# Performance work log

Hardware: AMD Instinct MI355X
Metric: run time of the kernel (lower is better)

## Reference

```python
import jax, jax.numpy as jnp
import numpy as np

N_NODES = 100000
N_EDGES = 1600000
N_GRAPHS = 1000
H = 128
F_IN = 128
F_EDGE = 16
DEPTH = 4


def setup_inputs() -> dict:
    key = jax.random.key(0)
    ks = jax.random.split(key, 10)
    s = 1.0 / np.sqrt(H)
    x = jax.random.normal(ks[0], (N_NODES, F_IN), dtype=jnp.float32)
    edge_index = jax.random.randint(ks[1], (2, N_EDGES), 0, N_NODES, dtype=jnp.int32)
    edge_attr = jax.random.normal(ks[2], (N_EDGES, F_EDGE), dtype=jnp.float32)
    batch = jnp.sort(jax.random.randint(ks[3], (N_NODES,), 0, N_GRAPHS, dtype=jnp.int32))
    W0 = jax.random.normal(ks[4], (F_IN, H), dtype=jnp.float32) * s
    b0 = jnp.zeros((H,), dtype=jnp.float32)
    W1 = jax.random.normal(ks[5], (DEPTH, H, H), dtype=jnp.float32) * s
    b1 = jnp.zeros((DEPTH, H), dtype=jnp.float32)
    W2 = jax.random.normal(ks[6], (DEPTH, H, H), dtype=jnp.float32) * s
    b2 = jnp.zeros((DEPTH, H), dtype=jnp.float32)
    Wf = jax.random.normal(ks[7], (H, 1), dtype=jnp.float32) * s
    bf = jnp.zeros((1,), dtype=jnp.float32)
    return {"x": x, "edge_index": edge_index, "edge_attr": edge_attr, "batch": batch,
            "W0": W0, "b0": b0, "W1": W1, "b1": b1, "W2": W2, "b2": b2, "Wf": Wf, "bf": bf}


def reference(x, edge_index, edge_attr, batch, W0, b0, W1, b1, W2, b2, Wf, bf):
    # edge_attr is read by the original forward but never used in the math.
    src, dst = edge_index[0], edge_index[1]
    n = x.shape[0]
    h0 = jax.nn.relu(x @ W0 + b0)  # [N, H]
    h = h0
    for i in range(DEPTH):
        # GINConv (eps=0): MLP(x + sum_{j in N(i)} x_j); messages flow src -> dst
        agg = jax.ops.segment_sum(h[src], dst, num_segments=n)  # [N, H]
        z = h + agg
        z = jax.nn.relu(z @ W1[i] + b1[i]) @ W2[i] + b2[i]
        # residual then relu (dropout p=0.02 is identity at eval)
        h = jax.nn.relu(z + h0)
    pooled = jax.ops.segment_sum(h, batch, num_segments=N_GRAPHS)  # [G, H]
    out = (pooled @ Wf + bf)[:, 0]  # [G]
    return out
```

## Files before the change

### kernel.cpp

```cpp
#include <hip/hip_runtime.h>

#define N_NODES 100000
#define N_EDGES 1600000
#define N_GRAPHS 1000
#define H 128
#define DEPTH 4
#define NB 391
#define BCAP 4864
#define WPITCH 136
#define WSLOT (H * WPITCH)

typedef __attribute__((ext_vector_type(8))) short bf16x8;
typedef __attribute__((ext_vector_type(4))) float f32x4;
typedef __attribute__((ext_vector_type(4))) unsigned int u32x4;

__device__ __forceinline__ unsigned short f2bf(float f) {
  unsigned int u = __float_as_uint(f);
  u += 0x7FFF + ((u >> 16) & 1);
  return (unsigned short)(u >> 16);
}
__device__ __forceinline__ float bflo(unsigned int v) { return __uint_as_float(v << 16); }
__device__ __forceinline__ float bfhi(unsigned int v) { return __uint_as_float(v & 0xFFFF0000u); }

__global__ __launch_bounds__(512) void k_bscan(const int* __restrict__ gcnt, int* __restrict__ boff) {
  __shared__ int sh[512];
  int t = threadIdx.x;
  int v = (t < NB) ? gcnt[t] : 0;
  sh[t] = v;
  __syncthreads();
  for (int s = 1; s < 512; s <<= 1) {
    int x = (t >= s) ? sh[t - s] : 0;
    __syncthreads();
    sh[t] += x;
    __syncthreads();
  }
  if (t < NB) boff[t] = sh[t] - v;
  if (t == 0) boff[NB] = N_EDGES;
}

__global__ __launch_bounds__(256) void k_bucket(const int* __restrict__ src, const int* __restrict__ dst,
                                                int* __restrict__ gcnt, unsigned int* __restrict__ ebuf) {
  __shared__ int cnt[NB];
  __shared__ int base[NB];
  int tid = threadIdx.x;
  int e0 = blockIdx.x * 4096;
  for (int i = tid; i < NB; i += 256) cnt[i] = 0;
  __syncthreads();
  unsigned int pk[16];
  int bk[16], rk[16];
#pragma unroll
  for (int i = 0; i < 16; ++i) {
    int e = e0 + i * 256 + tid;
    if (e < N_EDGES) {
      int s = src[e], d = dst[e];
      bk[i] = d >> 8;
      pk[i] = ((unsigned int)(d & 255) << 17) | (unsigned int)s;
      rk[i] = atomicAdd(&cnt[bk[i]], 1);
    } else
      bk[i] = -1;
  }
  __syncthreads();
  for (int i = tid; i < NB; i += 256)
    base[i] = cnt[i] ? atomicAdd(&gcnt[i], cnt[i]) : 0;
  __syncthreads();
#pragma unroll
  for (int i = 0; i < 16; ++i)
    if (bk[i] >= 0) ebuf[(size_t)bk[i] * BCAP + base[bk[i]] + rk[i]] = pk[i];
}

__global__ __launch_bounds__(256) void k_bsort(const unsigned int* __restrict__ ebuf,
                                               const int* __restrict__ gcnt, const int* __restrict__ boff,
                                               int* __restrict__ csr, int* __restrict__ offs) {
  __shared__ unsigned int arr[BCAP];
  __shared__ unsigned int srt[BCAP];
  __shared__ unsigned short rnk[BCAP];
  __shared__ int cnt[256];
  __shared__ int off[257];
  int b = blockIdx.x, tid = threadIdx.x;
  int beg = boff[b];
  int ce = min(gcnt[b], BCAP);
  cnt[tid] = 0;
  __syncthreads();
  for (int i = tid; i < ce; i += 256) {
    unsigned int p = ebuf[(size_t)b * BCAP + i];
    arr[i] = p;
    rnk[i] = (unsigned short)atomicAdd(&cnt[p >> 17], 1);
  }
  __syncthreads();
  int v = cnt[tid];
  off[tid + 1] = v;
  if (tid == 0) off[0] = 0;
  __syncthreads();
  for (int s = 1; s < 256; s <<= 1) {
    int x = (tid + 1 > s) ? off[tid + 1 - s] : 0;
    __syncthreads();
    off[tid + 1] += x;
    __syncthreads();
  }
  for (int i = tid; i < ce; i += 256) {
    unsigned int p = arr[i];
    srt[off[p >> 17] + rnk[i]] = p & 0x1FFFF;
  }
  __syncthreads();
  for (int i = tid; i < ce; i += 256) csr[beg + i] = (int)srt[i];
  int node = (b << 8) + tid;
  if (node < N_NODES) offs[node] = beg + off[tid];
  if (b == NB - 1 && tid == 0) offs[N_NODES] = N_EDGES;
}

__global__ __launch_bounds__(256) void k_wprep(const float* __restrict__ W0, const float* __restrict__ W1,
                                               const float* __restrict__ W2, unsigned short* __restrict__ wb) {
  int m = blockIdx.x >> 3, part = blockIdx.x & 7, tid = threadIdx.x;
  const float* src = (m == 0) ? W0 : ((m <= DEPTH) ? W1 + (size_t)(m - 1) * H * H : W2 + (size_t)(m - 1 - DEPTH) * H * H);
  unsigned short* dst = wb + (size_t)m * WSLOT;
  int idx = part * 256 + tid;
  int ng4 = idx & 31, kp = idx >> 5;
  float4 r0 = *(const float4*)&src[(2 * kp) * H + 4 * ng4];
  float4 r1 = *(const float4*)&src[(2 * kp + 1) * H + 4 * ng4];
  unsigned int p0 = (unsigned int)f2bf(r0.x) | ((unsigned int)f2bf(r1.x) << 16);
  unsigned int p1 = (unsigned int)f2bf(r0.y) | ((unsigned int)f2bf(r1.y) << 16);
  unsigned int p2 = (unsigned int)f2bf(r0.z) | ((unsigned int)f2bf(r1.z) << 16);
  unsigned int p3 = (unsigned int)f2bf(r0.w) | ((unsigned int)f2bf(r1.w) << 16);
  *(unsigned int*)&dst[(4 * ng4 + 0) * WPITCH + 2 * kp] = p0;
  *(unsigned int*)&dst[(4 * ng4 + 1) * WPITCH + 2 * kp] = p1;
  *(unsigned int*)&dst[(4 * ng4 + 2) * WPITCH + 2 * kp] = p2;
  *(unsigned int*)&dst[(4 * ng4 + 3) * WPITCH + 2 * kp] = p3;
}

__device__ __forceinline__ void stage_wb(const unsigned short* __restrict__ Wg, unsigned short* Wt, int tid) {
#pragma unroll
  for (int i = 0; i < 4; ++i) {
    int c = tid + i * 512;
    *(uint4*)&Wt[c * 8] = *(const uint4*)&Wg[c * 8];
  }
  int c = tid + 2048;
  if (c < 2176) *(uint4*)&Wt[c * 8] = *(const uint4*)&Wg[c * 8];
}

__global__ __launch_bounds__(512, 4) void k_lin(const float* __restrict__ in, const unsigned short* __restrict__ w0t,
                                                const float* __restrict__ bg, unsigned short* __restrict__ outp) {
  __shared__ __align__(16) unsigned short Wt[WSLOT];
  __shared__ __align__(16) unsigned short zs[128 * 136];
  int tid = threadIdx.x;
  int lane = tid & 63, w = tid >> 6;
  int q = lane >> 4, l16 = lane & 15;
  int n0 = blockIdx.x * 128;

  stage_wb(w0t, Wt, tid);

  int row = n0 + w * 16 + l16;
  int rr = (row < N_NODES) ? row : 0;
  bf16x8 afrag[4];
#pragma unroll
  for (int ks = 0; ks < 4; ++ks) {
    const float* p = &in[(size_t)rr * H + ks * 32 + q * 8];
    f32x4 f0 = __builtin_nontemporal_load((const f32x4*)p);
    f32x4 f1 = __builtin_nontemporal_load((const f32x4*)(p + 4));
    bf16x8 a;
    a[0] = (short)f2bf(f0.x); a[1] = (short)f2bf(f0.y); a[2] = (short)f2bf(f0.z); a[3] = (short)f2bf(f0.w);
    a[4] = (short)f2bf(f1.x); a[5] = (short)f2bf(f1.y); a[6] = (short)f2bf(f1.z); a[7] = (short)f2bf(f1.w);
    afrag[ks] = a;
  }
  f32x4 acc[8];
#pragma unroll
  for (int ct = 0; ct < 8; ++ct) acc[ct] = (f32x4){0.f, 0.f, 0.f, 0.f};
  __syncthreads();
#pragma unroll
  for (int ct = 0; ct < 8; ++ct)
#pragma unroll
    for (int ks = 0; ks < 4; ++ks) {
      bf16x8 b = *(bf16x8*)&Wt[(ct * 16 + l16) * WPITCH + ks * 32 + q * 8];
      acc[ct] = __builtin_amdgcn_mfma_f32_16x16x32_bf16(afrag[ks], b, acc[ct], 0, 0, 0);
    }
#pragma unroll
  for (int ct = 0; ct < 8; ++ct) {
    float bb = bg[ct * 16 + l16];
#pragma unroll
    for (int r = 0; r < 4; ++r) {
      float v = fmaxf(acc[ct][r] + bb, 0.f);
      zs[(w * 16 + q * 4 + r) * 136 + ct * 16 + l16] = f2bf(v);
    }
  }
  __syncthreads();
  int node = tid >> 2, cb = (tid & 3) * 32;
  if (n0 + node < N_NODES) {
#pragma unroll
    for (int i = 0; i < 4; ++i) {
      uint4 v = *(uint4*)&zs[node * 136 + cb + i * 8];
      *(uint4*)&outp[(size_t)(n0 + node) * H + cb + i * 8] = v;
    }
  }
}

#define ACC8(v)                                                       \
  {                                                                   \
    a0 += bflo(v.x); a1 += bfhi(v.x); a2 += bflo(v.y); a3 += bfhi(v.y); \
    a4 += bflo(v.z); a5 += bfhi(v.z); a6 += bflo(v.w); a7 += bfhi(v.w); \
  }

__global__ __launch_bounds__(512, 4) void k_mlp(const unsigned short* __restrict__ hin,
                                                const int* __restrict__ offs, const int* __restrict__ csr,
                                                const unsigned short* __restrict__ w1t, const float* __restrict__ b1g,
                                                const unsigned short* __restrict__ w2t, const float* __restrict__ b2g,
                                                const unsigned short* __restrict__ h0, unsigned short* __restrict__ hout) {
  __shared__ __align__(16) unsigned short Wt[WSLOT];
  __shared__ __align__(16) unsigned short zs[128 * 136];
  int tid = threadIdx.x;
  int n0 = blockIdx.x * 128;

  stage_wb(w1t, Wt, tid);

  {
    int g = tid >> 4, l = tid & 15;
    const uint4* hu4 = (const uint4*)hin;
    int bn = n0 + g * 4;
    int ofs[5];
#pragma unroll
    for (int k = 0; k < 5; ++k) ofs[k] = offs[min(bn + k, N_NODES)];
    int idxp[4];
#pragma unroll
    for (int it = 0; it < 4; ++it)
      idxp[it] = (ofs[it] + l < ofs[it + 1]) ? csr[ofs[it] + l] : N_NODES;
#pragma unroll
    for (int it = 0; it < 4; ++it) {
      int nl = g * 4 + it;
      int nc = min(n0 + nl, N_NODES);
      uint4 self = hu4[(size_t)nc * 16 + l];
      float a0 = bflo(self.x), a1 = bfhi(self.x), a2 = bflo(self.y), a3 = bfhi(self.y);
      float a4 = bflo(self.z), a5 = bfhi(self.z), a6 = bflo(self.w), a7 = bfhi(self.w);
      int beg = ofs[it], end = ofs[it + 1];
      int idx = idxp[it];
      for (int e = beg; e < end; e += 16) {
        int en = e + 16;
        int idxn = (en + l < end) ? csr[en + l] : N_NODES;
        int s[16];
#pragma unroll
        for (int j = 0; j < 16; ++j) s[j] = __shfl(idx, j, 16);
        uint4 v[16];
#pragma unroll
        for (int j = 0; j < 16; ++j) v[j] = hu4[(size_t)s[j] * 16 + l];
#pragma unroll
        for (int j = 0; j < 16; ++j) { ACC8(v[j]) }
        idx = idxn;
      }
      unsigned int o0 = (unsigned int)f2bf(a0) | ((unsigned int)f2bf(a1) << 16);
      unsigned int o1 = (unsigned int)f2bf(a2) | ((unsigned int)f2bf(a3) << 16);
      unsigned int o2 = (unsigned int)f2bf(a4) | ((unsigned int)f2bf(a5) << 16);
      unsigned int o3 = (unsigned int)f2bf(a6) | ((unsigned int)f2bf(a7) << 16);
      uint4 o;
      o.x = o0; o.y = o1; o.z = o2; o.w = o3;
      *(uint4*)&zs[nl * 136 + l * 8] = o;
    }
  }
  __syncthreads();

  int lane = tid & 63, w = tid >> 6;
  int q = lane >> 4, l16 = lane & 15;
  bf16x8 afrag[4];
#pragma unroll
  for (int ks = 0; ks < 4; ++ks)
    afrag[ks] = *(bf16x8*)&zs[(w * 16 + l16) * 136 + ks * 32 + q * 8];

  f32x4 acc[8];
#pragma unroll
  for (int ct = 0; ct < 8; ++ct) acc[ct] = (f32x4){0.f, 0.f, 0.f, 0.f};
#pragma unroll
  for (int ct = 0; ct < 8; ++ct)
#pragma unroll
    for (int ks = 0; ks < 4; ++ks) {
      bf16x8 b = *(bf16x8*)&Wt[(ct * 16 + l16) * WPITCH + ks * 32 + q * 8];
      acc[ct] = __builtin_amdgcn_mfma_f32_16x16x32_bf16(afrag[ks], b, acc[ct], 0, 0, 0);
    }
  __syncthreads();
  stage_wb(w2t, Wt, tid);
#pragma unroll
  for (int ct = 0; ct < 8; ++ct) {
    float bb = b1g[ct * 16 + l16];
#pragma unroll
    for (int r = 0; r < 4; ++r) {
      float v = fmaxf(acc[ct][r] + bb, 0.f);
      zs[(w * 16 + q * 4 + r) * 136 + ct * 16 + l16] = f2bf(v);
    }
  }
  __syncthreads();

  bf16x8 a2[4];
#pragma unroll
  for (int ks = 0; ks < 4; ++ks)
    a2[ks] = *(bf16x8*)&zs[(w * 16 + l16) * 136 + ks * 32 + q * 8];
  f32x4 acc2[8];
#pragma unroll
  for (int ct = 0; ct < 8; ++ct) acc2[ct] = (f32x4){0.f, 0.f, 0.f, 0.f};
#pragma unroll
  for (int ct = 0; ct < 8; ++ct)
#pragma unroll
    for (int ks = 0; ks < 4; ++ks) {
      bf16x8 b = *(bf16x8*)&Wt[(ct * 16 + l16) * WPITCH + ks * 32 + q * 8];
      acc2[ct] = __builtin_amdgcn_mfma_f32_16x16x32_bf16(a2[ks], b, acc2[ct], 0, 0, 0);
    }
#pragma unroll
  for (int ct = 0; ct < 8; ++ct) {
    float bb = b2g[ct * 16 + l16];
#pragma unroll
    for (int r = 0; r < 4; ++r) {
      float v = acc2[ct][r] + bb;
      zs[(w * 16 + q * 4 + r) * 136 + ct * 16 + l16] = f2bf(v);
    }
  }
  __syncthreads();
  int node = tid >> 2, cb = (tid & 3) * 32;
  if (n0 + node < N_NODES) {
    size_t base = (size_t)(n0 + node) * H + cb;
#pragma unroll
    for (int i = 0; i < 4; ++i) {
      u32x4 zv = *(u32x4*)&zs[node * 136 + cb + i * 8];
      u32x4 hv = *(const u32x4*)&h0[base + i * 8];
      u32x4 o;
#pragma unroll
      for (int j = 0; j < 4; ++j) {
        float a = fmaxf(bflo(zv[j]) + bflo(hv[j]), 0.f);
        float b = fmaxf(bfhi(zv[j]) + bfhi(hv[j]), 0.f);
        o[j] = (unsigned int)f2bf(a) | ((unsigned int)f2bf(b) << 16);
      }
      *(u32x4*)&hout[base + i * 8] = o;
    }
  }
}

__global__ void k_starts(const int* __restrict__ batch, int* __restrict__ starts) {
  int n = blockIdx.x * 256 + threadIdx.x;
  if (n >= N_NODES) return;
  int b = batch[n];
  if (n == 0) {
    for (int g = 0; g <= b; ++g) starts[g] = 0;
  } else {
    int bp = batch[n - 1];
    for (int g = bp + 1; g <= b; ++g) starts[g] = n;
  }
  if (n == N_NODES - 1) {
    for (int g = b + 1; g <= N_GRAPHS; ++g) starts[g] = N_NODES;
  }
}

__global__ __launch_bounds__(256) void k_pool(const unsigned short* __restrict__ h, const int* __restrict__ starts,
                                              const float* __restrict__ Wf, const float* __restrict__ bf_,
                                              float* __restrict__ out) {
  __shared__ float r[4];
  int g = blockIdx.x, tid = threadIdx.x;
  int lane = tid & 63, w = tid >> 6;
  int beg = starts[g], end = starts[g + 1];
  const unsigned int* hu = (const unsigned int*)h;
  float sx = 0.f, sy = 0.f;
  for (int n = beg + w; n < end; n += 4) {
    unsigned int v = hu[(size_t)n * 64 + lane];
    sx += bflo(v);
    sy += bfhi(v);
  }
  float val = sx * Wf[2 * lane] + sy * Wf[2 * lane + 1];
#pragma unroll
  for (int off = 32; off > 0; off >>= 1) val += __shfl_down(val, off);
  if (lane == 0) r[w] = val;
  __syncthreads();
  if (tid == 0) out[g] = r[0] + r[1] + r[2] + r[3] + bf_[0];
}

extern "C" void kernel_launch(void* const* d_in, const int* in_sizes, int n_in,
                              void* d_out, int out_size, void* d_ws, size_t ws_size,
                              hipStream_t stream) {
  const float* x = (const float*)d_in[0];
  const int* ei = (const int*)d_in[1];
  const int* srcv = ei;
  const int* dstv = ei + N_EDGES;
  const int* batch = (const int*)d_in[3];
  const float* W0 = (const float*)d_in[4];
  const float* b0 = (const float*)d_in[5];
  const float* W1 = (const float*)d_in[6];
  const float* b1 = (const float*)d_in[7];
  const float* W2 = (const float*)d_in[8];
  const float* b2 = (const float*)d_in[9];
  const float* Wf = (const float*)d_in[10];
  const float* bf_ = (const float*)d_in[11];
  float* out = (float*)d_out;

  char* ws = (char*)d_ws;
  size_t o = 0;
  auto alloc = [&](size_t bytes) {
    size_t r = o;
    o = (o + bytes + 255) & ~(size_t)255;
    return r;
  };
  int* offs = (int*)(ws + alloc((N_NODES + 1) * sizeof(int)));
  int* gcnt = (int*)(ws + alloc(NB * sizeof(int)));
  int* boff = (int*)(ws + alloc((NB + 1) * sizeof(int)));
  unsigned int* ebuf = (unsigned int*)(ws + alloc((size_t)NB * BCAP * 4));
  int* csr = (int*)(ws + alloc((size_t)N_EDGES * sizeof(int)));
  int* starts = (int*)(ws + alloc((N_GRAPHS + 1) * sizeof(int)));
  unsigned short* h0 = (unsigned short*)(ws + alloc((size_t)(N_NODES + 1) * H * 2));
  unsigned short* hA = (unsigned short*)(ws + alloc((size_t)(N_NODES + 1) * H * 2));
  unsigned short* hB = (unsigned short*)(ws + alloc((size_t)(N_NODES + 1) * H * 2));
  unsigned short* wbuf = (unsigned short*)(ws + alloc((size_t)9 * WSLOT * 2));

  (void)hipMemsetAsync(gcnt, 0, NB * sizeof(int), stream);
  (void)hipMemsetAsync(h0 + (size_t)N_NODES * H, 0, H * 2, stream);
  (void)hipMemsetAsync(hA + (size_t)N_NODES * H, 0, H * 2, stream);
  (void)hipMemsetAsync(hB + (size_t)N_NODES * H, 0, H * 2, stream);
  k_wprep<<<72, 256, 0, stream>>>(W0, W1, W2, wbuf);
  k_bucket<<<NB, 256, 0, stream>>>(srcv, dstv, gcnt, ebuf);
  k_bscan<<<1, 512, 0, stream>>>(gcnt, boff);
  k_bsort<<<NB, 256, 0, stream>>>(ebuf, gcnt, boff, csr, offs);
  k_starts<<<(N_NODES + 255) / 256, 256, 0, stream>>>(batch, starts);

  const int nblk = (N_NODES + 127) / 128;
  k_lin<<<nblk, 512, 0, stream>>>(x, wbuf, b0, h0);
  for (int i = 0; i < DEPTH; ++i) {
    const unsigned short* hin = (i == 0) ? h0 : ((i & 1) ? hA : hB);
    unsigned short* hout = (i & 1) ? hB : hA;
    k_mlp<<<nblk, 512, 0, stream>>>(hin, offs, csr,
                                    wbuf + (size_t)(1 + i) * WSLOT, b1 + (size_t)i * H,
                                    wbuf + (size_t)(1 + DEPTH + i) * WSLOT, b2 + (size_t)i * H,
                                    h0, hout);
  }
  k_pool<<<N_GRAPHS, 256, 0, stream>>>(hB, starts, Wf, bf_, out);
}
```

Measured before the change: 575.9 us.

## Split node features into column slices and separate aggregation from MLP kernel

Node feature buffers are stored as 8 column slices of 16 bf16 each, and neighbor aggregation moves into a separate k_agg kernel. Each k_agg block handles one slice for 64 nodes, so the gathered working set per slice (about 3.2 MB) can stay in cache across random neighbor reads. The MLP kernel then reads the aggregated z from global memory. This adds an extra round-trip of z through memory per layer and extra kernel launches, and gather reads shrink to 8 bytes per lane.

```diff
diff --git a/kernel.cpp b/kernel.cpp
--- a/kernel.cpp
+++ b/kernel.cpp
@@ -9,6 +9,8 @@
 #define BCAP 4864
 #define WPITCH 136
 #define WSLOT (H * WPITCH)
+#define NROW (N_NODES + 1)
+#define SLICE_STRIDE ((size_t)NROW * 16)
 
 typedef __attribute__((ext_vector_type(8))) short bf16x8;
 typedef __attribute__((ext_vector_type(4))) float f32x4;
@@ -127,6 +129,13 @@
   *(unsigned int*)&dst[(4 * ng4 + 3) * WPITCH + 2 * kp] = p3;
 }
 
+__global__ void k_zpad(unsigned short* __restrict__ h0, unsigned short* __restrict__ h) {
+  int t = threadIdx.x;
+  int s = (t >> 4) & 7, c = t & 15;
+  unsigned short* p = (t < 128) ? h0 : h;
+  p[(size_t)s * SLICE_STRIDE + (size_t)N_NODES * 16 + c] = 0;
+}
+
 __device__ __forceinline__ void stage_wb(const unsigned short* __restrict__ Wg, unsigned short* Wt, int tid) {
 #pragma unroll
   for (int i = 0; i < 4; ++i) {
@@ -187,83 +196,74 @@
 #pragma unroll
     for (int i = 0; i < 4; ++i) {
       uint4 v = *(uint4*)&zs[node * 136 + cb + i * 8];
-      *(uint4*)&outp[(size_t)(n0 + node) * H + cb + i * 8] = v;
-    }
-  }
-}
-
-#define ACC8(v)                                                       \
-  {                                                                   \
+      int sl = 2 * (tid & 3) + (i >> 1);
+      *(uint4*)&outp[(size_t)sl * SLICE_STRIDE + (size_t)(n0 + node) * 16 + (i & 1) * 8] = v;
+    }
+  }
+}
+
+#define ACC4(v)                                                         \
+  {                                                                     \
     a0 += bflo(v.x); a1 += bfhi(v.x); a2 += bflo(v.y); a3 += bfhi(v.y); \
-    a4 += bflo(v.z); a5 += bfhi(v.z); a6 += bflo(v.w); a7 += bfhi(v.w); \
-  }
-
-__global__ __launch_bounds__(512, 4) void k_mlp(const unsigned short* __restrict__ hin,
-                                                const int* __restrict__ offs, const int* __restrict__ csr,
+  }
+
+__global__ __launch_bounds__(256) void k_agg(const unsigned short* __restrict__ hin,
+                                             const int* __restrict__ offs, const int* __restrict__ csr,
+                                             unsigned short* __restrict__ z) {
+  int s = blockIdx.x & 7;
+  int node = (blockIdx.x >> 3) * 64 + (threadIdx.x >> 2);
+  int l = threadIdx.x & 3;
+  if (node >= N_NODES) return;
+  const uint2* hs = (const uint2*)(hin + (size_t)s * SLICE_STRIDE);
+  uint2 self = hs[(size_t)node * 4 + l];
+  float a0 = bflo(self.x), a1 = bfhi(self.x), a2 = bflo(self.y), a3 = bfhi(self.y);
+  int beg = offs[node], end = offs[node + 1];
+  for (int e = beg; e < end; e += 8) {
+    int c = end - e;
+    int i0 = (l < c) ? csr[e + l] : N_NODES;
+    int i1 = (4 + l < c) ? csr[e + 4 + l] : N_NODES;
+    int s0 = __shfl(i0, 0, 4), s1 = __shfl(i0, 1, 4), s2 = __shfl(i0, 2, 4), s3 = __shfl(i0, 3, 4);
+    int s4 = __shfl(i1, 0, 4), s5 = __shfl(i1, 1, 4), s6 = __shfl(i1, 2, 4), s7 = __shfl(i1, 3, 4);
+    uint2 v0 = hs[(size_t)s0 * 4 + l];
+    uint2 v1 = hs[(size_t)s1 * 4 + l];
+    uint2 v2 = hs[(size_t)s2 * 4 + l];
+    uint2 v3 = hs[(size_t)s3 * 4 + l];
+    uint2 v4 = hs[(size_t)s4 * 4 + l];
+    uint2 v5 = hs[(size_t)s5 * 4 + l];
+    uint2 v6 = hs[(size_t)s6 * 4 + l];
+    uint2 v7 = hs[(size_t)s7 * 4 + l];
+    ACC4(v0) ACC4(v1) ACC4(v2) ACC4(v3) ACC4(v4) ACC4(v5) ACC4(v6) ACC4(v7)
+  }
+  uint2 o;
+  o.x = (unsigned int)f2bf(a0) | ((unsigned int)f2bf(a1) << 16);
+  o.y = (unsigned int)f2bf(a2) | ((unsigned int)f2bf(a3) << 16);
+  *(uint2*)&z[(size_t)s * SLICE_STRIDE + (size_t)node * 16 + l * 4] = o;
+}
+
+__global__ __launch_bounds__(512, 4) void k_mlp(const unsigned short* __restrict__ zin,
                                                 const unsigned short* __restrict__ w1t, const float* __restrict__ b1g,
                                                 const unsigned short* __restrict__ w2t, const float* __restrict__ b2g,
                                                 const unsigned short* __restrict__ h0, unsigned short* __restrict__ hout) {
   __shared__ __align__(16) unsigned short Wt[WSLOT];
   __shared__ __align__(16) unsigned short zs[128 * 136];
   int tid = threadIdx.x;
-  int n0 = blockIdx.x * 128;
-
-  stage_wb(w1t, Wt, tid);
-
-  {
-    int g = tid >> 4, l = tid & 15;
-    const uint4* hu4 = (const uint4*)hin;
-    int bn = n0 + g * 4;
-    int ofs[5];
-#pragma unroll
-    for (int k = 0; k < 5; ++k) ofs[k] = offs[min(bn + k, N_NODES)];
-    int idxp[4];
-#pragma unroll
-    for (int it = 0; it < 4; ++it)
-      idxp[it] = (ofs[it] + l < ofs[it + 1]) ? csr[ofs[it] + l] : N_NODES;
-#pragma unroll
-    for (int it = 0; it < 4; ++it) {
-      int nl = g * 4 + it;
-      int nc = min(n0 + nl, N_NODES);
-      uint4 self = hu4[(size_t)nc * 16 + l];
-      float a0 = bflo(self.x), a1 = bfhi(self.x), a2 = bflo(self.y), a3 = bfhi(self.y);
-      float a4 = bflo(self.z), a5 = bfhi(self.z), a6 = bflo(self.w), a7 = bfhi(self.w);
-      int beg = ofs[it], end = ofs[it + 1];
-      int idx = idxp[it];
-      for (int e = beg; e < end; e += 16) {
-        int en = e + 16;
-        int idxn = (en + l < end) ? csr[en + l] : N_NODES;
-        int s[16];
-#pragma unroll
-        for (int j = 0; j < 16; ++j) s[j] = __shfl(idx, j, 16);
-        uint4 v[16];
-#pragma unroll
-        for (int j = 0; j < 16; ++j) v[j] = hu4[(size_t)s[j] * 16 + l];
-#pragma unroll
-        for (int j = 0; j < 16; ++j) { ACC8(v[j]) }
-        idx = idxn;
-      }
-      unsigned int o0 = (unsigned int)f2bf(a0) | ((unsigned int)f2bf(a1) << 16);
-      unsigned int o1 = (unsigned int)f2bf(a2) | ((unsigned int)f2bf(a3) << 16);
-      unsigned int o2 = (unsigned int)f2bf(a4) | ((unsigned int)f2bf(a5) << 16);
-      unsigned int o3 = (unsigned int)f2bf(a6) | ((unsigned int)f2bf(a7) << 16);
-      uint4 o;
-      o.x = o0; o.y = o1; o.z = o2; o.w = o3;
-      *(uint4*)&zs[nl * 136 + l * 8] = o;
-    }
-  }
-  __syncthreads();
-
   int lane = tid & 63, w = tid >> 6;
   int q = lane >> 4, l16 = lane & 15;
+  int n0 = blockIdx.x * 128;
+
+  stage_wb(w1t, Wt, tid);
+
+  int row = n0 + w * 16 + l16;
+  int rr = (row < N_NODES) ? row : 0;
   bf16x8 afrag[4];
 #pragma unroll
-  for (int ks = 0; ks < 4; ++ks)
-    afrag[ks] = *(bf16x8*)&zs[(w * 16 + l16) * 136 + ks * 32 + q * 8];
-
+  for (int ks = 0; ks < 4; ++ks) {
+    afrag[ks] = *(const bf16x8*)&zin[(size_t)(2 * ks + (q >> 1)) * SLICE_STRIDE + (size_t)rr * 16 + (q & 1) * 8];
+  }
   f32x4 acc[8];
 #pragma unroll
   for (int ct = 0; ct < 8; ++ct) acc[ct] = (f32x4){0.f, 0.f, 0.f, 0.f};
+  __syncthreads();
 #pragma unroll
   for (int ct = 0; ct < 8; ++ct)
 #pragma unroll
@@ -283,7 +283,6 @@
     }
   }
   __syncthreads();
-
   bf16x8 a2[4];
 #pragma unroll
   for (int ks = 0; ks < 4; ++ks)
@@ -310,11 +309,12 @@
   __syncthreads();
   int node = tid >> 2, cb = (tid & 3) * 32;
   if (n0 + node < N_NODES) {
-    size_t base = (size_t)(n0 + node) * H + cb;
 #pragma unroll
     for (int i = 0; i < 4; ++i) {
+      int sl = 2 * (tid & 3) + (i >> 1);
+      size_t base = (size_t)sl * SLICE_STRIDE + (size_t)(n0 + node) * 16 + (i & 1) * 8;
       u32x4 zv = *(u32x4*)&zs[node * 136 + cb + i * 8];
-      u32x4 hv = *(const u32x4*)&h0[base + i * 8];
+      u32x4 hv = *(const u32x4*)&h0[base];
       u32x4 o;
 #pragma unroll
       for (int j = 0; j < 4; ++j) {
@@ -322,7 +322,7 @@
         float b = fmaxf(bfhi(zv[j]) + bfhi(hv[j]), 0.f);
         o[j] = (unsigned int)f2bf(a) | ((unsigned int)f2bf(b) << 16);
       }
-      *(u32x4*)&hout[base + i * 8] = o;
+      *(u32x4*)&hout[base] = o;
     }
   }
 }
@@ -350,9 +350,10 @@
   int lane = tid & 63, w = tid >> 6;
   int beg = starts[g], end = starts[g + 1];
   const unsigned int* hu = (const unsigned int*)h;
+  size_t sbase = (size_t)(lane >> 3) * (SLICE_STRIDE / 2);
   float sx = 0.f, sy = 0.f;
   for (int n = beg + w; n < end; n += 4) {
-    unsigned int v = hu[(size_t)n * 64 + lane];
+    unsigned int v = hu[sbase + (size_t)n * 8 + (lane & 7)];
     sx += bflo(v);
     sy += bfhi(v);
   }
@@ -395,15 +396,13 @@
   unsigned int* ebuf = (unsigned int*)(ws + alloc((size_t)NB * BCAP * 4));
   int* csr = (int*)(ws + alloc((size_t)N_EDGES * sizeof(int)));
   int* starts = (int*)(ws + alloc((N_GRAPHS + 1) * sizeof(int)));
-  unsigned short* h0 = (unsigned short*)(ws + alloc((size_t)(N_NODES + 1) * H * 2));
-  unsigned short* hA = (unsigned short*)(ws + alloc((size_t)(N_NODES + 1) * H * 2));
-  unsigned short* hB = (unsigned short*)(ws + alloc((size_t)(N_NODES + 1) * H * 2));
+  unsigned short* h0 = (unsigned short*)(ws + alloc(8 * SLICE_STRIDE * 2));
+  unsigned short* h = (unsigned short*)(ws + alloc(8 * SLICE_STRIDE * 2));
+  unsigned short* z = (unsigned short*)(ws + alloc(8 * SLICE_STRIDE * 2));
   unsigned short* wbuf = (unsigned short*)(ws + alloc((size_t)9 * WSLOT * 2));
 
   (void)hipMemsetAsync(gcnt, 0, NB * sizeof(int), stream);
-  (void)hipMemsetAsync(h0 + (size_t)N_NODES * H, 0, H * 2, stream);
-  (void)hipMemsetAsync(hA + (size_t)N_NODES * H, 0, H * 2, stream);
-  (void)hipMemsetAsync(hB + (size_t)N_NODES * H, 0, H * 2, stream);
+  k_zpad<<<1, 256, 0, stream>>>(h0, h);
   k_wprep<<<72, 256, 0, stream>>>(W0, W1, W2, wbuf);
   k_bucket<<<NB, 256, 0, stream>>>(srcv, dstv, gcnt, ebuf);
   k_bscan<<<1, 512, 0, stream>>>(gcnt, boff);
@@ -411,14 +410,15 @@
   k_starts<<<(N_NODES + 255) / 256, 256, 0, stream>>>(batch, starts);
 
   const int nblk = (N_NODES + 127) / 128;
+  const int nagg = 8 * ((N_NODES + 63) / 64);
   k_lin<<<nblk, 512, 0, stream>>>(x, wbuf, b0, h0);
   for (int i = 0; i < DEPTH; ++i) {
-    const unsigned short* hin = (i == 0) ? h0 : ((i & 1) ? hA : hB);
-    unsigned short* hout = (i & 1) ? hB : hA;
-    k_mlp<<<nblk, 512, 0, stream>>>(hin, offs, csr,
+    const unsigned short* hin = (i == 0) ? h0 : h;
+    k_agg<<<nagg, 256, 0, stream>>>(hin, offs, csr, z);
+    k_mlp<<<nblk, 512, 0, stream>>>(z,
                                     wbuf + (size_t)(1 + i) * WSLOT, b1 + (size_t)i * H,
                                     wbuf + (size_t)(1 + DEPTH + i) * WSLOT, b2 + (size_t)i * H,
-                                    h0, hout);
-  }
-  k_pool<<<N_GRAPHS, 256, 0, stream>>>(hB, starts, Wf, bf_, out);
-}
+                                    h0, h);
+  }
+  k_pool<<<N_GRAPHS, 256, 0, stream>>>(h, starts, Wf, bf_, out);
+}
```

Measured after the change: 638.6 us. 10.9% more time.
